# Kernel optimization log

Hardware: AMD Instinct MI355X
Metric: run time of the kernel (lower is better)

## Reference

```python
import jax, jax.numpy as jnp
import numpy as np

B, N, M = 8, 4096, 2048
IN_DIM, D, CTX_DIM = 512, 512, 768


def setup_inputs() -> dict:
    key = jax.random.key(0)
    k_h, k_hr, k_c, k_a, k_k, k_v, k_o = jax.random.split(key, 7)
    s = 0.02  # init scale for weights
    return {
        "h": jax.random.normal(k_h, (B, N, IN_DIM), dtype=jnp.float32),
        "h_retrieved": jax.random.normal(k_hr, (B, M, CTX_DIM), dtype=jnp.float32),
        # torch nn.Linear convention: weight is [out_features, in_features]
        "W_cond": jax.random.normal(k_c, (IN_DIM, CTX_DIM), dtype=jnp.float32) * s,
        "W_attn": jax.random.normal(k_a, (D, IN_DIM), dtype=jnp.float32) * s,
        "W_k": jax.random.normal(k_k, (D, IN_DIM), dtype=jnp.float32) * s,
        "W_v": jax.random.normal(k_v, (D, IN_DIM), dtype=jnp.float32) * s,
        "W_out": jax.random.normal(k_o, (IN_DIM, D), dtype=jnp.float32) * s,
    }


def reference(h, h_retrieved, W_cond, W_attn, W_k, W_v, W_out):
    # cond_flag is True since context_dim != in_dim
    hr = h_retrieved @ W_cond.T                      # [B, M, in_dim]
    attn = jax.nn.softmax(h @ W_attn.T, axis=-1)     # [B, N, d], softmax over channel dim
    kv_in = jnp.concatenate([h, hr], axis=1)         # [B, N+M, in_dim]
    k = kv_in @ W_k.T                                # [B, N+M, d]
    v = kv_in @ W_v.T                                # [B, N+M, d]
    f = jnp.einsum('bnd,bne->bde', k, v)             # K^T V: [B, d, d]
    h_aug = jnp.einsum('bnd,bde->bne', attn, f)      # [B, N, d]
    return h + h_aug @ W_out.T                       # [B, N, in_dim]
```

## Files before the change

### kernel.cpp

```cpp
#include <hip/hip_runtime.h>
#include <hip/hip_bf16.h>


typedef unsigned short u16;
typedef __bf16 bf16x8 __attribute__((ext_vector_type(8)));
typedef float  f32x4  __attribute__((ext_vector_type(4)));
typedef float  f32v4  __attribute__((ext_vector_type(4)));
typedef u16    u16v4  __attribute__((ext_vector_type(4)));
typedef u16    u16v8  __attribute__((ext_vector_type(8)));

__device__ __forceinline__ u16 f2bf(float f) {
  unsigned u = __builtin_bit_cast(unsigned, f);
  u = u + 0x7FFFu + ((u >> 16) & 1u);
  return (u16)(u >> 16);
}
__device__ __forceinline__ float bf2f(u16 s) {
  return __builtin_bit_cast(float, (unsigned)s << 16);
}

__global__ __launch_bounds__(256) void cvt_T(const float* __restrict__ src,
                                             u16* __restrict__ dstT,
                                             long src_bs, long dstT_bs) {
  __shared__ u16 tile[64][72];
  long bz = blockIdx.z;
  const float* S = src + bz * src_bs;
  u16* DT = dstT + bz * dstT_bs;
  int r0 = blockIdx.x * 64;
  int c0 = blockIdx.y * 64;
  int t  = threadIdx.x;
  int tr = t >> 2;
  int tc = (t & 3) * 16;
  const float* sp = &S[(long)(r0 + tr) * 512 + c0 + tc];
#pragma unroll
  for (int q = 0; q < 2; ++q) {
    f32v4 a = *(const f32v4*)(sp + q * 8);
    f32v4 b = *(const f32v4*)(sp + q * 8 + 4);
    u16v8 o;
    o[0] = f2bf(a[0]); o[1] = f2bf(a[1]); o[2] = f2bf(a[2]); o[3] = f2bf(a[3]);
    o[4] = f2bf(b[0]); o[5] = f2bf(b[1]); o[6] = f2bf(b[2]); o[7] = f2bf(b[3]);
    *(u16v8*)&tile[tr][tc + q * 8] = o;
  }
  __syncthreads();
  int tr2 = t >> 3;
  int tc2 = (t & 7) * 8;
#pragma unroll
  for (int it = 0; it < 2; ++it) {
    int cr = it * 32 + tr2;
    u16v8 o;
#pragma unroll
    for (int j = 0; j < 8; ++j) o[j] = tile[tc2 + j][cr];
    *(u16v8*)&DT[(long)(c0 + cr) * 6144 + r0 + tc2] = o;
  }
}

__global__ __launch_bounds__(256) void prep_weights(
    const float* __restrict__ Wc, const float* __restrict__ Wa,
    const float* __restrict__ Wk, const float* __restrict__ Wv,
    const float* __restrict__ Wo,
    u16* __restrict__ wc, u16* __restrict__ wa, u16* __restrict__ wk,
    u16* __restrict__ wv, u16* __restrict__ wvT, u16* __restrict__ wo) {
  __shared__ u16 tile[64][72];
  int bx = blockIdx.x;
  int t = threadIdx.x;
  if (bx < 576) {
    const float* src; u16* dst; long base;
    if (bx < 192)      { src = Wc; dst = wc; base = (long)bx * 2048; }
    else if (bx < 320) { src = Wa; dst = wa; base = (long)(bx - 192) * 2048; }
    else if (bx < 448) { src = Wk; dst = wk; base = (long)(bx - 320) * 2048; }
    else               { src = Wo; dst = wo; base = (long)(bx - 448) * 2048; }
    long i = base + (long)t * 8;
    f32v4 a = *(const f32v4*)(src + i);
    f32v4 b = *(const f32v4*)(src + i + 4);
    u16v8 o;
    o[0] = f2bf(a[0]); o[1] = f2bf(a[1]); o[2] = f2bf(a[2]); o[3] = f2bf(a[3]);
    o[4] = f2bf(b[0]); o[5] = f2bf(b[1]); o[6] = f2bf(b[2]); o[7] = f2bf(b[3]);
    *(u16v8*)(dst + i) = o;
  } else {
    int b2 = bx - 576;
    int r0 = (b2 >> 3) * 64, c0 = (b2 & 7) * 64;
    int tr = t >> 2, tc = (t & 3) * 16;
    const float* sp = &Wv[(long)(r0 + tr) * 512 + c0 + tc];
#pragma unroll
    for (int q = 0; q < 2; ++q) {
      f32v4 a = *(const f32v4*)(sp + q * 8);
      f32v4 b = *(const f32v4*)(sp + q * 8 + 4);
      u16v8 o;
      o[0] = f2bf(a[0]); o[1] = f2bf(a[1]); o[2] = f2bf(a[2]); o[3] = f2bf(a[3]);
      o[4] = f2bf(b[0]); o[5] = f2bf(b[1]); o[6] = f2bf(b[2]); o[7] = f2bf(b[3]);
      *(u16v8*)&wv[(long)(r0 + tr) * 512 + c0 + tc + q * 8] = o;
      *(u16v8*)&tile[tr][tc + q * 8] = o;
    }
    __syncthreads();
    int tr2 = t >> 3, tc2 = (t & 7) * 8;
#pragma unroll
    for (int it = 0; it < 2; ++it) {
      int cr = it * 32 + tr2;
      u16v8 o;
#pragma unroll
      for (int j = 0; j < 8; ++j) o[j] = tile[tc2 + j][cr];
      *(u16v8*)&wvT[(long)(c0 + cr) * 512 + r0 + tc2] = o;
    }
  }
}

__global__ __launch_bounds__(256) void reduce8_bf16(const u16* __restrict__ parts,
                                                    u16* __restrict__ out) {
  long i = (((long)blockIdx.x * 256) + threadIdx.x) * 8;
  long b = i >> 18;
  long r = i & 262143;
  const u16* p = parts + b * 2097152 + r;
  float acc[8] = {};
#pragma unroll
  for (int s = 0; s < 8; ++s) {
    u16v8 v = *(const u16v8*)(p + (long)s * 262144);
#pragma unroll
    for (int j = 0; j < 8; ++j) acc[j] += bf2f(v[j]);
  }
  u16v8 o;
#pragma unroll
  for (int j = 0; j < 8; ++j) o[j] = f2bf(acc[j]);
  *(u16v8*)(out + i) = o;
}

template <int MODE>
__global__ __launch_bounds__(512, 2) void gemm256(
    const u16* __restrict__ A, const u16* __restrict__ B, void* __restrict__ Cout,
    const float* __restrict__ Res, int K, int lda, int ldb, int ldc,
    long sA, long sB, long sC, long sS, long sRes, int kslices) {
  __shared__ __align__(16) u16 lds[65536];

  int gx = gridDim.x, gy = gridDim.y;
  int nwg = gx * gy * (int)gridDim.z;
  int flat = blockIdx.x + gx * (blockIdx.y + gy * blockIdx.z);
  if ((nwg & 7) == 0) { int q = nwg >> 3; flat = (flat & 7) * q + (flat >> 3); }
  int bx = flat % gx; int tmp = flat / gx; int by = tmp % gy; int z = tmp / gy;
  int b = z / kslices;
  int s = z - b * kslices;

  long m0 = (long)bx * 256;
  long n0 = (long)by * 256;
  const u16* Ag = A + (long)b * sA + (long)s * K;
  const u16* Bg = B + (long)b * sB + (long)s * K;

  int tid  = threadIdx.x;
  int lane = tid & 63;
  int wid  = tid >> 6;
  int wm = wid >> 2;
  int wn = wid & 3;
  int l15 = lane & 15, l16 = lane >> 4, l7 = lane & 7;

  auto stage_half = [&](bool isA, int buf, int h, int ktile) {
    const u16* G = isA ? Ag : Bg;
    long rb = (isA ? m0 : n0) + h * 128;
    int ldg = isA ? lda : ldb;
    u16* base = lds + (isA ? 0 : 32768) + buf * 16384 + h * 8192;
    int row_lo = wid * 8 + (lane >> 3);
    int ce = ((lane & 7) ^ ((lane >> 3) & 7)) * 8;
#pragma unroll
    for (int q = 0; q < 2; ++q) {
      const u16* src = G + (rb + q * 64 + row_lo) * (long)ldg + ktile * 64 + ce;
      u16* dst = base + (q * 512 + wid * 64) * 8;
      __builtin_amdgcn_global_load_lds(
          (const __attribute__((address_space(1))) void*)src,
          (__attribute__((address_space(3))) void*)dst, 16, 0, 0);
    }
  };

  f32x4 acc[8][4] = {};
  int nk = K >> 6;

  stage_half(true,  0, 0, 0); stage_half(true,  0, 1, 0);
  stage_half(false, 0, 0, 0); stage_half(false, 0, 1, 0);

  for (int kt = 0; kt < nk; ++kt) {
    int cur = kt & 1, nxt = cur ^ 1;
    asm volatile("s_waitcnt vmcnt(0)\n\ts_barrier" ::: "memory");
    const u16* Ab = lds + cur * 16384 + wm * 8192;
    const u16* Bb = lds + 32768 + cur * 16384 + (wn >> 1) * 8192 + (wn & 1) * 4096;
    bool more = (kt + 1) < nk;
#pragma unroll
    for (int kk = 0; kk < 2; ++kk) {
      int csw = ((kk * 4 + l16) ^ l7) * 8;
      bf16x8 bf[4];
#pragma unroll
      for (int j = 0; j < 4; ++j)
        bf[j] = *(const bf16x8*)&Bb[(j * 16 + l15) * 64 + csw];
#pragma unroll
      for (int frh = 0; frh < 2; ++frh) {
        bf16x8 af[4];
#pragma unroll
        for (int i = 0; i < 4; ++i)
          af[i] = *(const bf16x8*)&Ab[((frh * 4 + i) * 16 + l15) * 64 + csw];
        if (more) {
          if (kk == 0 && frh == 0) {
            stage_half(true, nxt, 0, kt + 1); stage_half(true, nxt, 1, kt + 1);
          } else if (kk == 0 && frh == 1) {
            stage_half(false, nxt, 0, kt + 1); stage_half(false, nxt, 1, kt + 1);
          }
        }
        asm volatile("s_barrier" ::: "memory");
        __builtin_amdgcn_s_setprio(1);
#pragma unroll
        for (int i = 0; i < 4; ++i)
#pragma unroll
          for (int j = 0; j < 4; ++j)
            acc[frh * 4 + i][j] = __builtin_amdgcn_mfma_f32_16x16x32_bf16(
                af[i], bf[j], acc[frh * 4 + i][j], 0, 0, 0);
        __builtin_amdgcn_s_setprio(0);
        asm volatile("s_barrier" ::: "memory");
      }
    }
  }

  int lq = l16, lr = l15;
  float* ep = (float*)((char*)lds + wid * 4608);
  long cb  = (long)b * sC + (long)s * sS;
  int row0 = (int)m0 + wm * 128;
  int colb = (int)n0 + wn * 64;
#pragma unroll
  for (int fr = 0; fr < 8; ++fr) {
#pragma unroll
    for (int j = 0; j < 4; ++j)
#pragma unroll
      for (int r = 0; r < 4; ++r)
        ep[(lq * 4 + r) * 72 + lr + j * 16] = acc[fr][j][r];
#pragma unroll
    for (int p = 0; p < 4; ++p) {
      int rl = p * 4 + lq;
      f32x4 v = *(f32x4*)&ep[rl * 72 + lr * 4];
      long off = (long)(row0 + fr * 16 + rl) * ldc + colb + lr * 4;
      if (MODE == 0) {
        u16v4 o;
#pragma unroll
        for (int t2 = 0; t2 < 4; ++t2) o[t2] = f2bf(v[t2]);
        *(u16v4*)((u16*)Cout + cb + off) = o;
      } else {
        const float* R = Res + (long)b * sRes;
        f32v4 rv = *(const f32v4*)&R[off];
        f32v4 ov;
#pragma unroll
        for (int t2 = 0; t2 < 4; ++t2) ov[t2] = v[t2] + rv[t2];
        *(f32v4*)((float*)Cout + cb + off) = ov;
      }
    }
  }
}

template <int MODE, bool AF32>
__global__ __launch_bounds__(256) void gemm_nt(
    const void* __restrict__ Ap, const u16* __restrict__ B, void* __restrict__ Cout,
    const float* __restrict__ Res, int K, int lda, int ldb, int ldc,
    long sA, long sB, long sC, long sS, long sRes, int kslices) {
  __shared__ __align__(16) char smem_c[65536];

  int gx = gridDim.x, gy = gridDim.y;
  int nwg = gx * gy * (int)gridDim.z;
  int flat = blockIdx.x + gx * (blockIdx.y + gy * blockIdx.z);
  if ((nwg & 7) == 0) { int q = nwg >> 3; flat = (flat & 7) * q + (flat >> 3); }
  int bx = flat % gx; int tmp = flat / gx; int by = tmp % gy; int z = tmp / gy;

  int b = z / kslices;
  int s = z - b * kslices;

  long m0 = (long)bx * 128;
  long n0 = (long)by * 128;

  const u16* Ag = (const u16*)Ap + (long)b * sA + (long)s * K;
  const float* Af = (const float*)Ap + (long)b * sA;
  const u16* Bg = B + (long)b * sB + (long)s * K;

  int tid  = threadIdx.x;
  int lane = tid & 63;
  int wid  = tid >> 6;
  int wm = wid >> 1, wn = wid & 1;

  int srow = wid * 8 + (lane >> 3);
  int scol = (lane & 7) * 8;
  int arow  = tid >> 1;
  int acolb = (tid & 1) * 32;

  auto stageA = [&](u16* Asd, int k0) {
#pragma unroll
    for (int c = 0; c < 4; ++c) {
      int row = c * 32 + srow;
      __builtin_amdgcn_global_load_lds(
          (const __attribute__((address_space(1))) void*)(Ag + (m0 + row) * lda + k0 + scol),
          (__attribute__((address_space(3))) void*)(Asd + (c * 32 + wid * 8) * 64),
          16, 0, 0);
    }
  };
  auto stageB = [&](u16* Bsd, int k0) {
#pragma unroll
    for (int c = 0; c < 4; ++c) {
      int row = c * 32 + srow;
      __builtin_amdgcn_global_load_lds(
          (const __attribute__((address_space(1))) void*)(Bg + (n0 + row) * ldb + k0 + scol),
          (__attribute__((address_space(3))) void*)(Bsd + (c * 32 + wid * 8) * 64),
          16, 0, 0);
    }
  };
  f32v4 xr[8];
  auto loadA = [&](int k0) {
    const float* sp = Af + (m0 + arow) * (long)lda + k0 + acolb;
#pragma unroll
    for (int q = 0; q < 8; ++q) xr[q] = *(const f32v4*)(sp + q * 4);
  };
  auto cvtA = [&](u16* Asd) {
#pragma unroll
    for (int q = 0; q < 4; ++q) {
      u16v8 o;
      o[0] = f2bf(xr[2*q][0]); o[1] = f2bf(xr[2*q][1]);
      o[2] = f2bf(xr[2*q][2]); o[3] = f2bf(xr[2*q][3]);
      o[4] = f2bf(xr[2*q+1][0]); o[5] = f2bf(xr[2*q+1][1]);
      o[6] = f2bf(xr[2*q+1][2]); o[7] = f2bf(xr[2*q+1][3]);
      *(u16v8*)&Asd[arow * 64 + acolb + q * 8] = o;
    }
  };

  f32x4 acc[4][4] = {};
  int nk = K >> 6;

  if constexpr (AF32) {
    loadA(0);
    cvtA((u16*)smem_c);
    asm volatile("s_waitcnt lgkmcnt(0)" ::: "memory");
  } else {
    stageA((u16*)smem_c, 0);
  }
  stageB((u16*)(smem_c + 32768), 0);

  for (int t = 0; t < nk; ++t) {
    u16* Asc = (u16*)(smem_c + (t & 1) * 16384);
    u16* Bsc = (u16*)(smem_c + 32768 + (t & 1) * 16384);
    u16* Asn = (u16*)(smem_c + ((t + 1) & 1) * 16384);
    u16* Bsn = (u16*)(smem_c + 32768 + ((t + 1) & 1) * 16384);
    bool more = (t + 1) < nk;
    if (more) {
      if constexpr (AF32) {
        loadA((t + 1) * 64);
        stageB(Bsn, (t + 1) * 64);
        asm volatile("s_waitcnt vmcnt(12)\n\ts_barrier" ::: "memory");
      } else {
        stageA(Asn, (t + 1) * 64);
        stageB(Bsn, (t + 1) * 64);
        asm volatile("s_waitcnt vmcnt(8)\n\ts_barrier" ::: "memory");
      }
    } else {
      asm volatile("s_waitcnt vmcnt(0)\n\ts_barrier" ::: "memory");
    }
#pragma unroll
    for (int kk = 0; kk < 2; ++kk) {
      int kofs = kk * 32 + (lane >> 4) * 8;
      bf16x8 af[4], bfr[4];
#pragma unroll
      for (int i = 0; i < 4; ++i) {
        af[i]  = *(const bf16x8*)&Asc[(wm * 64 + i * 16 + (lane & 15)) * 64 + kofs];
        bfr[i] = *(const bf16x8*)&Bsc[(wn * 64 + i * 16 + (lane & 15)) * 64 + kofs];
      }
#pragma unroll
      for (int i = 0; i < 4; ++i)
#pragma unroll
        for (int j = 0; j < 4; ++j)
          acc[i][j] = __builtin_amdgcn_mfma_f32_16x16x32_bf16(af[i], bfr[j], acc[i][j], 0, 0, 0);
    }
    if constexpr (AF32) {
      if (more) cvtA(Asn);
      asm volatile("s_waitcnt lgkmcnt(0)\n\ts_barrier" ::: "memory");
    } else {
      asm volatile("s_barrier" ::: "memory");
    }
  }

  long cb = (long)b * sC + (long)s * sS;
  int lq = lane >> 4;
  int lr = lane & 15;

  if constexpr (MODE == 3) {
    u16* tT = (u16*)smem_c;
#pragma unroll
    for (int i = 0; i < 4; ++i)
#pragma unroll
      for (int j = 0; j < 4; ++j)
#pragma unroll
        for (int r = 0; r < 4; ++r)
          tT[(wn * 64 + j * 16 + lr) * 136 + wm * 64 + i * 16 + lq * 4 + r] =
              f2bf(acc[i][j][r]);
    __syncthreads();
    int ct   = tid >> 1;
    int half = (tid & 1) * 64;
    u16* dst = (u16*)Cout + cb + (long)(n0 + ct) * ldc + m0 + half;
    const u16* srcl = &tT[ct * 136 + half];
#pragma unroll
    for (int q = 0; q < 8; ++q)
      *(u16v8*)(dst + q * 8) = *(const u16v8*)(srcl + q * 8);
  } else {
    float* ep = (float*)(smem_c + wid * 4608);
    int row0 = (int)m0 + wm * 64;
    int colb = (int)n0 + wn * 64;
#pragma unroll
    for (int i = 0; i < 4; ++i) {
#pragma unroll
      for (int j = 0; j < 4; ++j)
#pragma unroll
        for (int r = 0; r < 4; ++r)
          ep[(lq * 4 + r) * 72 + lr + j * 16] = acc[i][j][r];
#pragma unroll
      for (int p = 0; p < 4; ++p) {
        int rl = p * 4 + lq;
        f32x4 v = *(f32x4*)&ep[rl * 72 + lr * 4];
        long off = (long)(row0 + i * 16 + rl) * ldc + colb + lr * 4;
        u16v4 o;
#pragma unroll
        for (int t2 = 0; t2 < 4; ++t2) o[t2] = f2bf(v[t2]);
        *(u16v4*)((u16*)Cout + cb + off) = o;
      }
    }
  }
}

__global__ __launch_bounds__(256) void gemm64(
    const u16* __restrict__ A, const u16* __restrict__ B, u16* __restrict__ Cout,
    int K, int lda, int ldb, int ldc, long sA, long sB, long sC) {
  __shared__ __align__(16) char smem_c[49152];

  int gx = gridDim.x, gy = gridDim.y;
  int nwg = gx * gy * (int)gridDim.z;
  int flat = blockIdx.x + gx * (blockIdx.y + gy * blockIdx.z);
  if ((nwg & 7) == 0) { int q = nwg >> 3; flat = (flat & 7) * q + (flat >> 3); }
  int bx = flat % gx; int tmp = flat / gx; int by = tmp % gy; int b = tmp / gy;

  long n0 = (long)bx * 128;
  long m0 = (long)by * 64;
  const u16* Ag = A + (long)b * sA;
  const u16* Bg = B + (long)b * sB;

  int tid  = threadIdx.x;
  int lane = tid & 63;
  int wid  = tid >> 6;
  int wm = wid >> 1, wn = wid & 1;

  int srow = wid * 8 + (lane >> 3);
  int scol = (lane & 7) * 8;

  auto stageA = [&](u16* Asd, int k0) {
#pragma unroll
    for (int c = 0; c < 2; ++c) {
      int row = c * 32 + srow;
      __builtin_amdgcn_global_load_lds(
          (const __attribute__((address_space(1))) void*)(Ag + (m0 + row) * lda + k0 + scol),
          (__attribute__((address_space(3))) void*)(Asd + (c * 32 + wid * 8) * 64),
          16, 0, 0);
    }
  };
  auto stageB = [&](u16* Bsd, int k0) {
#pragma unroll
    for (int c = 0; c < 4; ++c) {
      int row = c * 32 + srow;
      __builtin_amdgcn_global_load_lds(
          (const __attribute__((address_space(1))) void*)(Bg + (n0 + row) * ldb + k0 + scol),
          (__attribute__((address_space(3))) void*)(Bsd + (c * 32 + wid * 8) * 64),
          16, 0, 0);
    }
  };

  f32x4 acc[2][4] = {};
  int nk = K >> 6;

  stageA((u16*)smem_c, 0);
  stageB((u16*)(smem_c + 16384), 0);

  for (int t = 0; t < nk; ++t) {
    u16* Asc = (u16*)(smem_c + (t & 1) * 8192);
    u16* Bsc = (u16*)(smem_c + 16384 + (t & 1) * 16384);
    u16* Asn = (u16*)(smem_c + ((t + 1) & 1) * 8192);
    u16* Bsn = (u16*)(smem_c + 16384 + ((t + 1) & 1) * 16384);
    bool more = (t + 1) < nk;
    if (more) {
      stageA(Asn, (t + 1) * 64);
      stageB(Bsn, (t + 1) * 64);
      asm volatile("s_waitcnt vmcnt(6)\n\ts_barrier" ::: "memory");
    } else {
      asm volatile("s_waitcnt vmcnt(0)\n\ts_barrier" ::: "memory");
    }
#pragma unroll
    for (int kk = 0; kk < 2; ++kk) {
      int kofs = kk * 32 + (lane >> 4) * 8;
      bf16x8 af[2], bfr[4];
#pragma unroll
      for (int i = 0; i < 2; ++i)
        af[i]  = *(const bf16x8*)&Asc[(wm * 32 + i * 16 + (lane & 15)) * 64 + kofs];
#pragma unroll
      for (int j = 0; j < 4; ++j)
        bfr[j] = *(const bf16x8*)&Bsc[(wn * 64 + j * 16 + (lane & 15)) * 64 + kofs];
#pragma unroll
      for (int i = 0; i < 2; ++i)
#pragma unroll
        for (int j = 0; j < 4; ++j)
          acc[i][j] = __builtin_amdgcn_mfma_f32_16x16x32_bf16(af[i], bfr[j], acc[i][j], 0, 0, 0);
    }
    asm volatile("s_barrier" ::: "memory");
  }

  int lq = lane >> 4;
  int lr = lane & 15;
  float* ep = (float*)(smem_c + wid * 4608);
  long cb  = (long)b * sC;
  int row0 = (int)m0 + wm * 32;
  int colb = (int)n0 + wn * 64;
#pragma unroll
  for (int i = 0; i < 2; ++i) {
#pragma unroll
    for (int j = 0; j < 4; ++j)
#pragma unroll
      for (int r = 0; r < 4; ++r)
        ep[(lq * 4 + r) * 72 + lr + j * 16] = acc[i][j][r];
#pragma unroll
    for (int p = 0; p < 4; ++p) {
      int rl = p * 4 + lq;
      f32x4 v = *(f32x4*)&ep[rl * 72 + lr * 4];
      long off = (long)(row0 + i * 16 + rl) * ldc + colb + lr * 4;
      u16v4 o;
#pragma unroll
      for (int t2 = 0; t2 < 4; ++t2) o[t2] = f2bf(v[t2]);
      *(u16v4*)(Cout + cb + off) = o;
    }
  }
}

__global__ __launch_bounds__(256, 2) void gemm_sm(
    const float* __restrict__ A,
    const u16* __restrict__ Bw,
    u16* __restrict__ C) {
  __shared__ __align__(16) char smem[73728];
  u16* As = (u16*)smem;
  u16* Bs = (u16*)(smem + 8192);

  int nwg = gridDim.x;
  int flat = blockIdx.x;
  if ((nwg & 7) == 0) { int q = nwg >> 3; flat = (flat & 7) * q + (flat >> 3); }
  long m0 = (long)flat * 64;

  int tid = threadIdx.x;
  int lane = tid & 63;
  int wid = tid >> 6;

  int srow = wid * 8 + (lane >> 3);
  int scol = (lane & 7) * 8;
  int arow  = tid >> 2;
  int acolb = (tid & 3) * 16;

  f32x4 acc[4][8] = {};

  for (int k0 = 0; k0 < 512; k0 += 64) {
    const float* sp = A + (m0 + arow) * 512 + k0 + acolb;
    f32v4 x0 = *(const f32v4*)sp;
    f32v4 x1 = *(const f32v4*)(sp + 4);
    f32v4 x2 = *(const f32v4*)(sp + 8);
    f32v4 x3 = *(const f32v4*)(sp + 12);
#pragma unroll
    for (int c = 0; c < 16; ++c) {
      int row = c * 32 + srow;
      __builtin_amdgcn_global_load_lds(
          (const __attribute__((address_space(1))) void*)(Bw + (long)row * 512 + k0 + scol),
          (__attribute__((address_space(3))) void*)(Bs + (c * 32 + wid * 8) * 64),
          16, 0, 0);
    }
    u16v8 o0, o1;
    o0[0] = f2bf(x0[0]); o0[1] = f2bf(x0[1]); o0[2] = f2bf(x0[2]); o0[3] = f2bf(x0[3]);
    o0[4] = f2bf(x1[0]); o0[5] = f2bf(x1[1]); o0[6] = f2bf(x1[2]); o0[7] = f2bf(x1[3]);
    o1[0] = f2bf(x2[0]); o1[1] = f2bf(x2[1]); o1[2] = f2bf(x2[2]); o1[3] = f2bf(x2[3]);
    o1[4] = f2bf(x3[0]); o1[5] = f2bf(x3[1]); o1[6] = f2bf(x3[2]); o1[7] = f2bf(x3[3]);
    *(u16v8*)&As[arow * 64 + acolb] = o0;
    *(u16v8*)&As[arow * 64 + acolb + 8] = o1;
    __syncthreads();
#pragma unroll
    for (int kk = 0; kk < 2; ++kk) {
      int kofs = kk * 32 + (lane >> 4) * 8;
      bf16x8 af[4], bfr[8];
#pragma unroll
      for (int i = 0; i < 4; ++i)
        af[i] = *(const bf16x8*)&As[(i * 16 + (lane & 15)) * 64 + kofs];
#pragma unroll
      for (int j = 0; j < 8; ++j)
        bfr[j] = *(const bf16x8*)&Bs[(wid * 128 + j * 16 + (lane & 15)) * 64 + kofs];
#pragma unroll
      for (int i = 0; i < 4; ++i)
#pragma unroll
        for (int j = 0; j < 8; ++j)
          acc[i][j] = __builtin_amdgcn_mfma_f32_16x16x32_bf16(af[i], bfr[j], acc[i][j], 0, 0, 0);
    }
    __syncthreads();
  }

  int lq = lane >> 4, lr = lane & 15;
  float* sm = (float*)smem;
  float* ss = (float*)(smem + 1024);

#pragma unroll
  for (int i = 0; i < 4; ++i)
#pragma unroll
    for (int r = 0; r < 4; ++r) {
      float m = acc[i][0][r];
#pragma unroll
      for (int j = 1; j < 8; ++j) m = fmaxf(m, acc[i][j][r]);
#pragma unroll
      for (int o = 1; o < 16; o <<= 1) m = fmaxf(m, __shfl_xor(m, o, 16));
      if (lr == 0) sm[(i * 16 + lq * 4 + r) * 4 + wid] = m;
    }
  __syncthreads();
  float rinv[4][4];
#pragma unroll
  for (int i = 0; i < 4; ++i)
#pragma unroll
    for (int r = 0; r < 4; ++r) {
      f32v4 g4 = *(const f32v4*)&sm[(i * 16 + lq * 4 + r) * 4];
      float gm = fmaxf(fmaxf(g4[0], g4[1]), fmaxf(g4[2], g4[3]));
      float s = 0.f;
#pragma unroll
      for (int j = 0; j < 8; ++j) {
        float e = __expf(acc[i][j][r] - gm);
        acc[i][j][r] = e;
        s += e;
      }
#pragma unroll
      for (int o = 1; o < 16; o <<= 1) s += __shfl_xor(s, o, 16);
      if (lr == 0) ss[(i * 16 + lq * 4 + r) * 4 + wid] = s;
    }
  __syncthreads();
#pragma unroll
  for (int i = 0; i < 4; ++i)
#pragma unroll
    for (int r = 0; r < 4; ++r) {
      f32v4 g4 = *(const f32v4*)&ss[(i * 16 + lq * 4 + r) * 4];
      rinv[i][r] = 1.0f / (g4[0] + g4[1] + g4[2] + g4[3]);
    }
  __syncthreads();

  float* ep = (float*)(smem + wid * 4608);
#pragma unroll
  for (int i = 0; i < 4; ++i) {
#pragma unroll
    for (int jh = 0; jh < 2; ++jh) {
#pragma unroll
      for (int j = 0; j < 4; ++j)
#pragma unroll
        for (int r = 0; r < 4; ++r)
          ep[(lq * 4 + r) * 72 + lr + j * 16] = acc[i][jh * 4 + j][r] * rinv[i][r];
#pragma unroll
      for (int p = 0; p < 4; ++p) {
        int rl = p * 4 + lq;
        f32x4 v = *(f32x4*)&ep[rl * 72 + lr * 4];
        u16v4 o;
#pragma unroll
        for (int t = 0; t < 4; ++t) o[t] = f2bf(v[t]);
        *(u16v4*)&C[(m0 + i * 16 + rl) * 512 + wid * 128 + jh * 64 + lr * 4] = o;
      }
    }
  }
}

extern "C" void kernel_launch(void* const* d_in, const int* in_sizes, int n_in,
                              void* d_out, int out_size, void* d_ws, size_t ws_size,
                              hipStream_t stream) {
  (void)in_sizes; (void)n_in; (void)out_size; (void)ws_size;
  const float* h    = (const float*)d_in[0];
  const float* hret = (const float*)d_in[1];
  const float* Wc   = (const float*)d_in[2];
  const float* Wa   = (const float*)d_in[3];
  const float* Wk   = (const float*)d_in[4];
  const float* Wv   = (const float*)d_in[5];
  const float* Wo   = (const float*)d_in[6];
  float* out = (float*)d_out;
  char*  ws  = (char*)d_ws;

  constexpr long MB = 1024 * 1024;
  u16*   w_cond = (u16*)(ws + 0);
  u16*   w_attn = (u16*)(ws + 786432);
  u16*   w_k    = (u16*)(ws + 1310720);
  u16*   w_v    = (u16*)(ws + 1835008);
  u16*   w_out  = (u16*)(ws + 2359296);
  u16*   w_vT   = (u16*)(ws + 2883584);
  u16*   gparts = (u16*)(ws + 4 * MB);
  u16*   attn   = (u16*)(ws + 36 * MB);
  u16*   g_bf   = (u16*)(ws + 68 * MB);
  u16*   u_mat  = (u16*)(ws + 72 * MB);
  u16*   v1     = (u16*)(ws + 73 * MB);
  u16*   f2t    = (u16*)(ws + 77 * MB);
  u16*   xt     = (u16*)(ws + 84 * MB);

  cvt_T<<<dim3(64, 8, 8), 256, 0, stream>>>(h, xt, 2097152L, 3145728L);
  prep_weights<<<640, 256, 0, stream>>>(Wc, Wa, Wk, Wv, Wo,
      w_cond, w_attn, w_k, w_v, w_vT, w_out);

  gemm_nt<3, true><<<dim3(16, 4, 8), 256, 0, stream>>>(hret, w_cond, xt + 4096, nullptr,
      768, 768, 768, 6144, 1572864L, 0, 3145728L, 0, 0, 1);

  gemm_sm<<<512, 256, 0, stream>>>(h, w_attn, attn);

  gemm256<0><<<dim3(2, 2, 64), 512, 0, stream>>>(xt, xt, gparts, nullptr,
      768, 6144, 6144, 512, 3145728L, 3145728L, 2097152L, 262144L, 0, 8);
  reduce8_bf16<<<1024, 256, 0, stream>>>(gparts, g_bf);

  gemm64<<<dim3(4, 8, 1), 256, 0, stream>>>(w_out, w_vT, u_mat,
      512, 512, 512, 512, 0, 0, 0);
  gemm64<<<dim3(4, 8, 8), 256, 0, stream>>>(u_mat, g_bf, v1,
      512, 512, 512, 512, 0, 262144L, 262144L);
  gemm64<<<dim3(4, 8, 8), 256, 0, stream>>>(v1, w_k, f2t,
      512, 512, 512, 512, 262144L, 0, 262144L);

  gemm256<1><<<dim3(16, 2, 8), 512, 0, stream>>>(attn, f2t, out, h,
      512, 512, 512, 512, 2097152L, 262144L, 2097152L, 0, 2097152L, 1);
}
```

Measured before the change: 200.3 us.

## Pre-convert h_retrieved to bf16 and swap GEMM operands to drop transposed epilogue

Adds a separate elementwise kernel that converts h_retrieved from fp32 to bf16 in workspace, placed where gparts is later written. The conditioning GEMM now takes W_cond as A and the bf16 h_retrieved as B. Its output therefore comes out already transposed, so the in-loop fp32 load/convert path and the LDS transpose epilogue are removed. In exchange it adds an extra launch plus a write and re-read of a 24MB bf16 buffer.

```diff
diff --git a/kernel.cpp b/kernel.cpp
--- a/kernel.cpp
+++ b/kernel.cpp
@@ -16,6 +16,18 @@
 }
 __device__ __forceinline__ float bf2f(u16 s) {
   return __builtin_bit_cast(float, (unsigned)s << 16);
+}
+
+__global__ __launch_bounds__(256) void cvt_f32_bf16(const float* __restrict__ in,
+                                                    u16* __restrict__ out, long n) {
+  long i = (((long)blockIdx.x * 256) + threadIdx.x) * 8;
+  if (i >= n) return;
+  f32v4 a = *(const f32v4*)(in + i);
+  f32v4 b = *(const f32v4*)(in + i + 4);
+  u16v8 o;
+  o[0] = f2bf(a[0]); o[1] = f2bf(a[1]); o[2] = f2bf(a[2]); o[3] = f2bf(a[3]);
+  o[4] = f2bf(b[0]); o[5] = f2bf(b[1]); o[6] = f2bf(b[2]); o[7] = f2bf(b[3]);
+  *(u16v8*)(out + i) = o;
 }
 
 __global__ __launch_bounds__(256) void cvt_T(const float* __restrict__ src,
@@ -246,28 +258,21 @@
   }
 }
 
-template <int MODE, bool AF32>
 __global__ __launch_bounds__(256) void gemm_nt(
-    const void* __restrict__ Ap, const u16* __restrict__ B, void* __restrict__ Cout,
-    const float* __restrict__ Res, int K, int lda, int ldb, int ldc,
-    long sA, long sB, long sC, long sS, long sRes, int kslices) {
+    const u16* __restrict__ A, const u16* __restrict__ B, u16* __restrict__ Cout,
+    int K, int lda, int ldb, int ldc, long sA, long sB, long sC) {
   __shared__ __align__(16) char smem_c[65536];
 
   int gx = gridDim.x, gy = gridDim.y;
   int nwg = gx * gy * (int)gridDim.z;
   int flat = blockIdx.x + gx * (blockIdx.y + gy * blockIdx.z);
   if ((nwg & 7) == 0) { int q = nwg >> 3; flat = (flat & 7) * q + (flat >> 3); }
-  int bx = flat % gx; int tmp = flat / gx; int by = tmp % gy; int z = tmp / gy;
-
-  int b = z / kslices;
-  int s = z - b * kslices;
+  int bx = flat % gx; int tmp = flat / gx; int by = tmp % gy; int b = tmp / gy;
 
   long m0 = (long)bx * 128;
   long n0 = (long)by * 128;
-
-  const u16* Ag = (const u16*)Ap + (long)b * sA + (long)s * K;
-  const float* Af = (const float*)Ap + (long)b * sA;
-  const u16* Bg = B + (long)b * sB + (long)s * K;
+  const u16* Ag = A + (long)b * sA;
+  const u16* Bg = B + (long)b * sB;
 
   int tid  = threadIdx.x;
   int lane = tid & 63;
@@ -276,8 +281,6 @@
 
   int srow = wid * 8 + (lane >> 3);
   int scol = (lane & 7) * 8;
-  int arow  = tid >> 1;
-  int acolb = (tid & 1) * 32;
 
   auto stageA = [&](u16* Asd, int k0) {
 #pragma unroll
@@ -299,52 +302,22 @@
           16, 0, 0);
     }
   };
-  f32v4 xr[8];
-  auto loadA = [&](int k0) {
-    const float* sp = Af + (m0 + arow) * (long)lda + k0 + acolb;
-#pragma unroll
-    for (int q = 0; q < 8; ++q) xr[q] = *(const f32v4*)(sp + q * 4);
-  };
-  auto cvtA = [&](u16* Asd) {
-#pragma unroll
-    for (int q = 0; q < 4; ++q) {
-      u16v8 o;
-      o[0] = f2bf(xr[2*q][0]); o[1] = f2bf(xr[2*q][1]);
-      o[2] = f2bf(xr[2*q][2]); o[3] = f2bf(xr[2*q][3]);
-      o[4] = f2bf(xr[2*q+1][0]); o[5] = f2bf(xr[2*q+1][1]);
-      o[6] = f2bf(xr[2*q+1][2]); o[7] = f2bf(xr[2*q+1][3]);
-      *(u16v8*)&Asd[arow * 64 + acolb + q * 8] = o;
-    }
-  };
 
   f32x4 acc[4][4] = {};
   int nk = K >> 6;
 
-  if constexpr (AF32) {
-    loadA(0);
-    cvtA((u16*)smem_c);
-    asm volatile("s_waitcnt lgkmcnt(0)" ::: "memory");
-  } else {
-    stageA((u16*)smem_c, 0);
-  }
+  stageA((u16*)smem_c, 0);
   stageB((u16*)(smem_c + 32768), 0);
 
   for (int t = 0; t < nk; ++t) {
     u16* Asc = (u16*)(smem_c + (t & 1) * 16384);
     u16* Bsc = (u16*)(smem_c + 32768 + (t & 1) * 16384);
-    u16* Asn = (u16*)(smem_c + ((t + 1) & 1) * 16384);
-    u16* Bsn = (u16*)(smem_c + 32768 + ((t + 1) & 1) * 16384);
-    bool more = (t + 1) < nk;
-    if (more) {
-      if constexpr (AF32) {
-        loadA((t + 1) * 64);
-        stageB(Bsn, (t + 1) * 64);
-        asm volatile("s_waitcnt vmcnt(12)\n\ts_barrier" ::: "memory");
-      } else {
-        stageA(Asn, (t + 1) * 64);
-        stageB(Bsn, (t + 1) * 64);
-        asm volatile("s_waitcnt vmcnt(8)\n\ts_barrier" ::: "memory");
-      }
+    if (t + 1 < nk) {
+      u16* Asn = (u16*)(smem_c + ((t + 1) & 1) * 16384);
+      u16* Bsn = (u16*)(smem_c + 32768 + ((t + 1) & 1) * 16384);
+      stageA(Asn, (t + 1) * 64);
+      stageB(Bsn, (t + 1) * 64);
+      asm volatile("s_waitcnt vmcnt(8)\n\ts_barrier" ::: "memory");
     } else {
       asm volatile("s_waitcnt vmcnt(0)\n\ts_barrier" ::: "memory");
     }
@@ -363,57 +336,32 @@
         for (int j = 0; j < 4; ++j)
           acc[i][j] = __builtin_amdgcn_mfma_f32_16x16x32_bf16(af[i], bfr[j], acc[i][j], 0, 0, 0);
     }
-    if constexpr (AF32) {
-      if (more) cvtA(Asn);
-      asm volatile("s_waitcnt lgkmcnt(0)\n\ts_barrier" ::: "memory");
-    } else {
-      asm volatile("s_barrier" ::: "memory");
-    }
-  }
-
-  long cb = (long)b * sC + (long)s * sS;
+    asm volatile("s_barrier" ::: "memory");
+  }
+
+  float* ep = (float*)(smem_c + wid * 4608);
+  long cb  = (long)b * sC;
+  int row0 = (int)m0 + wm * 64;
+  int colb = (int)n0 + wn * 64;
   int lq = lane >> 4;
   int lr = lane & 15;
 
-  if constexpr (MODE == 3) {
-    u16* tT = (u16*)smem_c;
-#pragma unroll
-    for (int i = 0; i < 4; ++i)
-#pragma unroll
-      for (int j = 0; j < 4; ++j)
-#pragma unroll
-        for (int r = 0; r < 4; ++r)
-          tT[(wn * 64 + j * 16 + lr) * 136 + wm * 64 + i * 16 + lq * 4 + r] =
-              f2bf(acc[i][j][r]);
-    __syncthreads();
-    int ct   = tid >> 1;
-    int half = (tid & 1) * 64;
-    u16* dst = (u16*)Cout + cb + (long)(n0 + ct) * ldc + m0 + half;
-    const u16* srcl = &tT[ct * 136 + half];
-#pragma unroll
-    for (int q = 0; q < 8; ++q)
-      *(u16v8*)(dst + q * 8) = *(const u16v8*)(srcl + q * 8);
-  } else {
-    float* ep = (float*)(smem_c + wid * 4608);
-    int row0 = (int)m0 + wm * 64;
-    int colb = (int)n0 + wn * 64;
-#pragma unroll
-    for (int i = 0; i < 4; ++i) {
-#pragma unroll
-      for (int j = 0; j < 4; ++j)
-#pragma unroll
-        for (int r = 0; r < 4; ++r)
-          ep[(lq * 4 + r) * 72 + lr + j * 16] = acc[i][j][r];
-#pragma unroll
-      for (int p = 0; p < 4; ++p) {
-        int rl = p * 4 + lq;
-        f32x4 v = *(f32x4*)&ep[rl * 72 + lr * 4];
-        long off = (long)(row0 + i * 16 + rl) * ldc + colb + lr * 4;
-        u16v4 o;
-#pragma unroll
-        for (int t2 = 0; t2 < 4; ++t2) o[t2] = f2bf(v[t2]);
-        *(u16v4*)((u16*)Cout + cb + off) = o;
-      }
+#pragma unroll
+  for (int i = 0; i < 4; ++i) {
+#pragma unroll
+    for (int j = 0; j < 4; ++j)
+#pragma unroll
+      for (int r = 0; r < 4; ++r)
+        ep[(lq * 4 + r) * 72 + lr + j * 16] = acc[i][j][r];
+#pragma unroll
+    for (int p = 0; p < 4; ++p) {
+      int rl = p * 4 + lq;
+      f32x4 v = *(f32x4*)&ep[rl * 72 + lr * 4];
+      long off = (long)(row0 + i * 16 + rl) * ldc + colb + lr * 4;
+      u16v4 o;
+#pragma unroll
+      for (int t2 = 0; t2 < 4; ++t2) o[t2] = f2bf(v[t2]);
+      *(u16v4*)(Cout + cb + off) = o;
     }
   }
 }
@@ -674,26 +622,28 @@
   char*  ws  = (char*)d_ws;
 
   constexpr long MB = 1024 * 1024;
-  u16*   w_cond = (u16*)(ws + 0);
-  u16*   w_attn = (u16*)(ws + 786432);
-  u16*   w_k    = (u16*)(ws + 1310720);
-  u16*   w_v    = (u16*)(ws + 1835008);
-  u16*   w_out  = (u16*)(ws + 2359296);
-  u16*   w_vT   = (u16*)(ws + 2883584);
-  u16*   gparts = (u16*)(ws + 4 * MB);
-  u16*   attn   = (u16*)(ws + 36 * MB);
-  u16*   g_bf   = (u16*)(ws + 68 * MB);
-  u16*   u_mat  = (u16*)(ws + 72 * MB);
-  u16*   v1     = (u16*)(ws + 73 * MB);
-  u16*   f2t    = (u16*)(ws + 77 * MB);
-  u16*   xt     = (u16*)(ws + 84 * MB);
+  u16*   w_cond  = (u16*)(ws + 0);
+  u16*   w_attn  = (u16*)(ws + 786432);
+  u16*   w_k     = (u16*)(ws + 1310720);
+  u16*   w_v     = (u16*)(ws + 1835008);
+  u16*   w_out   = (u16*)(ws + 2359296);
+  u16*   w_vT    = (u16*)(ws + 2883584);
+  u16*   hret_bf = (u16*)(ws + 4 * MB);
+  u16*   gparts  = (u16*)(ws + 4 * MB);
+  u16*   attn    = (u16*)(ws + 36 * MB);
+  u16*   g_bf    = (u16*)(ws + 68 * MB);
+  u16*   u_mat   = (u16*)(ws + 72 * MB);
+  u16*   v1      = (u16*)(ws + 73 * MB);
+  u16*   f2t     = (u16*)(ws + 77 * MB);
+  u16*   xt      = (u16*)(ws + 84 * MB);
 
   cvt_T<<<dim3(64, 8, 8), 256, 0, stream>>>(h, xt, 2097152L, 3145728L);
   prep_weights<<<640, 256, 0, stream>>>(Wc, Wa, Wk, Wv, Wo,
       w_cond, w_attn, w_k, w_v, w_vT, w_out);
-
-  gemm_nt<3, true><<<dim3(16, 4, 8), 256, 0, stream>>>(hret, w_cond, xt + 4096, nullptr,
-      768, 768, 768, 6144, 1572864L, 0, 3145728L, 0, 0, 1);
+  cvt_f32_bf16<<<6144, 256, 0, stream>>>(hret, hret_bf, 12582912L);
+
+  gemm_nt<<<dim3(4, 16, 8), 256, 0, stream>>>(w_cond, hret_bf, xt + 4096,
+      768, 768, 768, 6144, 0, 1572864L, 3145728L);
 
   gemm_sm<<<512, 256, 0, stream>>>(h, w_attn, attn);
 
```

Measured after the change: 197.2 us. About the same (-1.6%).
